# Optimization experiments

Measured on AMD Instinct MI355X. Metric: run time of the kernel, lower is better.

## Reference

```python
import jax, jax.numpy as jnp
import numpy as np

UNITS = 1024
INPUT_DIM = 512
BATCH = 2048

def setup_inputs() -> dict:
    key = jax.random.key(0)
    k1, k2, k3, k4 = jax.random.split(key, 4)
    return {
        "inputs": jax.random.normal(k1, (BATCH, INPUT_DIM), dtype=jnp.float32),
        "h_tm1": jax.random.normal(k2, (BATCH, UNITS), dtype=jnp.float32),
        "c_tm1": jax.random.normal(k3, (BATCH, UNITS), dtype=jnp.float32),
        # keras 'random_normal' initializer: stddev 0.05
        "kernel": jax.random.normal(k4, (UNITS + INPUT_DIM, 4 * UNITS), dtype=jnp.float32) * 0.05,
    }

def reference(inputs, h_tm1, c_tm1, kernel):
    # z = concat([h, x]) @ kernel ; kernel rows: [units (h-block); input_dim (x-block)]
    z = jnp.concatenate([h_tm1, inputs], axis=-1) @ kernel  # [B, 4*units]
    z0, z1, z2, z3 = jnp.split(z, 4, axis=-1)
    i = jax.nn.sigmoid(z0)
    f = jax.nn.sigmoid(z1)
    c_tilde = jnp.tanh(z2)
    o = jax.nn.sigmoid(z3)
    c = f * c_tm1 + i * c_tilde
    h = o * jnp.tanh(c)
    return (h, c)
```

## Files before the change

kernel.cpp:

```cpp
#include <hip/hip_runtime.h>
#include <hip/hip_bf16.h>
#include <stdint.h>

#define UNITS 1024
#define IDIM  512
#define BATCH 2048
#define KTOT  1536
#define NGATE 4096
#define BK    64
#define NITER (KTOT / BK)

typedef short bf16x8 __attribute__((ext_vector_type(8)));
typedef float f32x4  __attribute__((ext_vector_type(4)));

#define AS3(p) ((__attribute__((address_space(3))) void*)(p))
#define AS1(p) ((const __attribute__((address_space(1))) void*)(p))

union P8 { bf16x8 v; __hip_bfloat16 e[8]; };

#define NBLK_A 1536
#define NBLK_T 3072

__global__ __launch_bounds__(256) void prep(
    const float* __restrict__ x, const float* __restrict__ h,
    const float* __restrict__ W,
    __hip_bfloat16* __restrict__ A, __hip_bfloat16* __restrict__ Wt) {
  __shared__ float tile[32][65];
  const int tid = threadIdx.x;
  if (blockIdx.x < NBLK_A) {
    const int id = blockIdx.x * 256 + tid;
    const int r = id / (KTOT / 8);
    const int k = (id % (KTOT / 8)) * 8;
    const float* src = (k < UNITS) ? h + (size_t)r * UNITS + k
                                   : x + (size_t)r * IDIM + (k - UNITS);
    const float4 v0 = ((const float4*)src)[0];
    const float4 v1 = ((const float4*)src)[1];
    P8 o;
    o.e[0] = __float2bfloat16(v0.x); o.e[1] = __float2bfloat16(v0.y);
    o.e[2] = __float2bfloat16(v0.z); o.e[3] = __float2bfloat16(v0.w);
    o.e[4] = __float2bfloat16(v1.x); o.e[5] = __float2bfloat16(v1.y);
    o.e[6] = __float2bfloat16(v1.z); o.e[7] = __float2bfloat16(v1.w);
    *(bf16x8*)(A + (size_t)r * KTOT + k) = o.v;
  } else {
    const int b  = blockIdx.x - NBLK_A;
    const int kb = b >> 7;
    const int nb = b & 127;
    const int k0 = kb * 64, n0 = nb * 32;
    const int n4 = (tid & 7) * 4;
    const int kk = tid >> 3;
#pragma unroll
    for (int rr = 0; rr < 64; rr += 32) {
      const float4 v = *(const float4*)(W + (size_t)(k0 + kk + rr) * NGATE + n0 + n4);
      tile[n4 + 0][kk + rr] = v.x; tile[n4 + 1][kk + rr] = v.y;
      tile[n4 + 2][kk + rr] = v.z; tile[n4 + 3][kk + rr] = v.w;
    }
    __syncthreads();
    const int n  = tid >> 3;
    const int k8 = (tid & 7) * 8;
    P8 o;
#pragma unroll
    for (int j = 0; j < 8; ++j) o.e[j] = __float2bfloat16(tile[n][k8 + j]);
    *(bf16x8*)(Wt + (size_t)(n0 + n) * KTOT + k0 + k8) = o.v;
  }
}

__global__ __launch_bounds__(256, 2) void lstm_gemm(
    const __hip_bfloat16* __restrict__ A,
    const __hip_bfloat16* __restrict__ Wt,
    const float* __restrict__ c_tm1,
    float* __restrict__ out) {
  __shared__ __attribute__((aligned(128))) char lds[4 * 16384];

  const int tid  = threadIdx.x;
  const int w    = tid >> 6;
  const int lane = tid & 63;
  const int quad = lane >> 4;
  const int m16  = lane & 15;
  const int wr   = w >> 1;
  const int wu   = w & 1;

  const int mb = blockIdx.x >> 5;
  const int ub = blockIdx.x & 31;
  const int m0 = mb * 128;
  const int u0 = ub * 32;

  const __hip_bfloat16* ptr[8];
  int dst[8];
#pragma unroll
  for (int s = 0; s < 8; ++s) {
    const int q  = s * 4 + w;
    const int ci = (q & 15) * 64 + lane;
    const int row = ci >> 3;
    const int k8  = (ci & 7) ^ (row & 7);
    if (q < 16) {
      ptr[s] = A + (size_t)(m0 + row) * KTOT + k8 * 8;
      dst[s] = q * 1024;
    } else {
      const int wrow = ((row >> 5) << 10) + u0 + (row & 31);
      ptr[s] = Wt + (size_t)wrow * KTOT + k8 * 8;
      dst[s] = 32768 + (q - 16) * 1024;
    }
  }

  f32x4 acc[4][4];
#pragma unroll
  for (int i = 0; i < 4; ++i)
#pragma unroll
    for (int g = 0; g < 4; ++g) {
      f32x4 z = {0.f, 0.f, 0.f, 0.f};
      acc[i][g] = z;
    }

#pragma unroll
  for (int s = 0; s < 8; ++s)
    __builtin_amdgcn_global_load_lds(AS1(ptr[s]), AS3(lds + dst[s]), 16, 0, 0);
  __syncthreads();

  for (int it = 0; it < NITER; ++it) {
    const int cur = it & 1;
    const int nxt = cur ^ 1;
    if (it < NITER - 1) {
      const int koff = (it + 1) * BK;
#pragma unroll
      for (int s = 0; s < 8; ++s)
        __builtin_amdgcn_global_load_lds(AS1(ptr[s] + koff),
                                         AS3(lds + dst[s] + nxt * 16384), 16, 0, 0);
    }
    const char* abuf = lds + cur * 16384;
    const char* bbuf = lds + 32768 + cur * 16384;
#pragma unroll
    for (int t = 0; t < 2; ++t) {
      bf16x8 a[4], b[4];
#pragma unroll
      for (int i = 0; i < 4; ++i) {
        const int row  = wr * 64 + i * 16 + m16;
        const int slot = (t * 4 + quad) ^ (row & 7);
        a[i] = *(const bf16x8*)(abuf + (row * 8 + slot) * 16);
      }
#pragma unroll
      for (int g = 0; g < 4; ++g) {
        const int vr   = g * 32 + wu * 16 + m16;
        const int slot = (t * 4 + quad) ^ (vr & 7);
        b[g] = *(const bf16x8*)(bbuf + (vr * 8 + slot) * 16);
      }
#pragma unroll
      for (int g = 0; g < 4; ++g)
#pragma unroll
        for (int i = 0; i < 4; ++i)
          acc[i][g] = __builtin_amdgcn_mfma_f32_16x16x32_bf16(a[i], b[g], acc[i][g], 0, 0, 0);
    }
    __syncthreads();
  }

  const int u = u0 + wu * 16 + m16;
#pragma unroll
  for (int i = 0; i < 4; ++i)
#pragma unroll
    for (int reg = 0; reg < 4; ++reg) {
      const int r = m0 + wr * 64 + i * 16 + quad * 4 + reg;
      const float z0 = acc[i][0][reg];
      const float z1 = acc[i][1][reg];
      const float z2 = acc[i][2][reg];
      const float z3 = acc[i][3][reg];
      const float ig = 1.f / (1.f + __expf(-z0));
      const float fg = 1.f / (1.f + __expf(-z1));
      const float ct = 1.f - 2.f / (__expf(2.f * z2) + 1.f);
      const float og = 1.f / (1.f + __expf(-z3));
      const float cc = fg * c_tm1[(size_t)r * UNITS + u] + ig * ct;
      const float hh = og * (1.f - 2.f / (__expf(2.f * cc) + 1.f));
      out[(size_t)r * UNITS + u] = hh;
      out[(size_t)BATCH * UNITS + (size_t)r * UNITS + u] = cc;
    }
}

__global__ __launch_bounds__(256) void lstm_naive(
    const float* __restrict__ x, const float* __restrict__ h,
    const float* __restrict__ c_tm1, const float* __restrict__ W,
    float* __restrict__ out) {
  int idx = blockIdx.x * 256 + threadIdx.x;
  int r = idx / UNITS;
  int u = idx % UNITS;
  float z[4] = {0.f, 0.f, 0.f, 0.f};
  for (int k = 0; k < KTOT; ++k) {
    float a = (k < UNITS) ? h[(size_t)r * UNITS + k] : x[(size_t)r * IDIM + k - UNITS];
#pragma unroll
    for (int g = 0; g < 4; ++g)
      z[g] += a * W[(size_t)k * NGATE + g * UNITS + u];
  }
  float ig = 1.f / (1.f + __expf(-z[0]));
  float fg = 1.f / (1.f + __expf(-z[1]));
  float ct = 1.f - 2.f / (__expf(2.f * z[2]) + 1.f);
  float og = 1.f / (1.f + __expf(-z[3]));
  float cc = fg * c_tm1[(size_t)r * UNITS + u] + ig * ct;
  float hh = og * (1.f - 2.f / (__expf(2.f * cc) + 1.f));
  out[(size_t)r * UNITS + u] = hh;
  out[(size_t)BATCH * UNITS + (size_t)r * UNITS + u] = cc;
}

extern "C" void kernel_launch(void* const* d_in, const int* in_sizes, int n_in,
                              void* d_out, int out_size, void* d_ws, size_t ws_size,
                              hipStream_t stream) {
  const float* x = (const float*)d_in[0];
  const float* h = (const float*)d_in[1];
  const float* c = (const float*)d_in[2];
  const float* W = (const float*)d_in[3];
  float* out = (float*)d_out;

  const size_t needA  = (size_t)BATCH * KTOT * sizeof(__hip_bfloat16);
  const size_t needWt = (size_t)NGATE * KTOT * sizeof(__hip_bfloat16);
  if (ws_size < needA + needWt) {
    hipLaunchKernelGGL(lstm_naive, dim3((BATCH * UNITS) / 256), dim3(256), 0, stream,
                       x, h, c, W, out);
    return;
  }

  __hip_bfloat16* A  = (__hip_bfloat16*)d_ws;
  __hip_bfloat16* Wt = (__hip_bfloat16*)((char*)d_ws + needA);

  hipLaunchKernelGGL(prep, dim3(NBLK_A + NBLK_T), dim3(256), 0, stream, x, h, W, A, Wt);
  hipLaunchKernelGGL(lstm_gemm, dim3(512), dim3(256), 0, stream, A, Wt, c, out);
}
```

Measured before the change: 120.8 us.

## Split K-tile into half-stages with vmcnt waits, new swizzle, prefetch c_tm1

The 64-wide K tile is split into two 32-wide halves in LDS with a 4-slot XOR swizzle. Loads are issued per half, and partial s_waitcnt vmcnt plus barriers replace the full __syncthreads, so the next half-tile's loads overlap the MFMAs on the current half. MFMA sections are wrapped in s_setprio, and the c_tm1 values for the epilogue are loaded before the final compute steps to hide their latency. The hand-written waitcnt counts and the LDS buffer reuse make correctness depend on exact load ordering.

```diff
diff --git a/kernel.cpp b/kernel.cpp
--- a/kernel.cpp
+++ b/kernel.cpp
@@ -84,23 +84,37 @@
   const int m0 = mb * 128;
   const int u0 = ub * 32;
 
-  const __hip_bfloat16* ptr[8];
-  int dst[8];
-#pragma unroll
-  for (int s = 0; s < 8; ++s) {
+  const __hip_bfloat16* ptr[4];
+  int dst[4];
+#pragma unroll
+  for (int s = 0; s < 4; ++s) {
     const int q  = s * 4 + w;
-    const int ci = (q & 15) * 64 + lane;
-    const int row = ci >> 3;
-    const int k8  = (ci & 7) ^ (row & 7);
-    if (q < 16) {
+    const int ci = (q & 7) * 64 + lane;
+    const int row = ci >> 2;
+    const int sl  = ci & 3;
+    const int xs  = (row & 3) ^ ((row >> 2) & 3);
+    const int k8  = sl ^ xs;
+    if (q < 8) {
       ptr[s] = A + (size_t)(m0 + row) * KTOT + k8 * 8;
       dst[s] = q * 1024;
     } else {
       const int wrow = ((row >> 5) << 10) + u0 + (row & 31);
       ptr[s] = Wt + (size_t)wrow * KTOT + k8 * 8;
-      dst[s] = 32768 + (q - 16) * 1024;
-    }
-  }
+      dst[s] = 32768 + (q - 8) * 1024;
+    }
+  }
+
+  auto issue = [&](int koffE, int ldsOff) {
+#pragma unroll
+    for (int s = 0; s < 4; ++s)
+      __builtin_amdgcn_global_load_lds(AS1(ptr[s] + koffE),
+                                       AS3(lds + dst[s] + ldsOff), 16, 0, 0);
+  };
+
+  const int x16  = (m16 & 3) ^ ((m16 >> 2) & 3);
+  const int sA   = quad ^ x16;
+  const int aoff = (wr * 64 + m16) * 64 + sA * 16;
+  const int boff = 32768 + (wu * 16 + m16) * 64 + sA * 16;
 
   f32x4 acc[4][4];
 #pragma unroll
@@ -111,48 +125,59 @@
       acc[i][g] = z;
     }
 
-#pragma unroll
-  for (int s = 0; s < 8; ++s)
-    __builtin_amdgcn_global_load_lds(AS1(ptr[s]), AS3(lds + dst[s]), 16, 0, 0);
-  __syncthreads();
-
-  for (int it = 0; it < NITER; ++it) {
-    const int cur = it & 1;
-    const int nxt = cur ^ 1;
-    if (it < NITER - 1) {
-      const int koff = (it + 1) * BK;
-#pragma unroll
-      for (int s = 0; s < 8; ++s)
-        __builtin_amdgcn_global_load_lds(AS1(ptr[s] + koff),
-                                         AS3(lds + dst[s] + nxt * 16384), 16, 0, 0);
-    }
-    const char* abuf = lds + cur * 16384;
-    const char* bbuf = lds + 32768 + cur * 16384;
-#pragma unroll
-    for (int t = 0; t < 2; ++t) {
-      bf16x8 a[4], b[4];
-#pragma unroll
-      for (int i = 0; i < 4; ++i) {
-        const int row  = wr * 64 + i * 16 + m16;
-        const int slot = (t * 4 + quad) ^ (row & 7);
-        a[i] = *(const bf16x8*)(abuf + (row * 8 + slot) * 16);
-      }
-#pragma unroll
-      for (int g = 0; g < 4; ++g) {
-        const int vr   = g * 32 + wu * 16 + m16;
-        const int slot = (t * 4 + quad) ^ (vr & 7);
-        b[g] = *(const bf16x8*)(bbuf + (vr * 8 + slot) * 16);
-      }
-#pragma unroll
-      for (int g = 0; g < 4; ++g)
-#pragma unroll
-        for (int i = 0; i < 4; ++i)
-          acc[i][g] = __builtin_amdgcn_mfma_f32_16x16x32_bf16(a[i], b[g], acc[i][g], 0, 0, 0);
-    }
-    __syncthreads();
+  auto compute = [&](int coff) {
+    bf16x8 a[4], b[4];
+    const char* ab = lds + coff + aoff;
+    const char* bb = lds + coff + boff;
+#pragma unroll
+    for (int i = 0; i < 4; ++i) a[i] = *(const bf16x8*)(ab + i * 1024);
+#pragma unroll
+    for (int g = 0; g < 4; ++g) b[g] = *(const bf16x8*)(bb + g * 2048);
+    __builtin_amdgcn_s_setprio(1);
+#pragma unroll
+    for (int g = 0; g < 4; ++g)
+#pragma unroll
+      for (int i = 0; i < 4; ++i)
+        acc[i][g] = __builtin_amdgcn_mfma_f32_16x16x32_bf16(a[i], b[g], acc[i][g], 0, 0, 0);
+    __builtin_amdgcn_s_setprio(0);
+  };
+
+#define WAITB(N)                                          \
+  asm volatile("s_waitcnt vmcnt(" #N ")" ::: "memory");   \
+  __builtin_amdgcn_s_barrier();                           \
+  asm volatile("" ::: "memory");
+
+  issue(0, 0);
+  issue(32, 8192);
+
+  for (int it = 0; it < NITER - 1; ++it) {
+    const int coff = (it & 1) * 16384;
+    const int noff = coff ^ 16384;
+    const int ke   = (it + 1) * BK;
+    issue(ke, noff);
+    WAITB(8)
+    issue(ke + 32, noff + 8192);
+    compute(coff);
+    WAITB(8)
+    compute(coff + 8192);
   }
 
   const int u = u0 + wu * 16 + m16;
+  float cpre[4][4];
+#pragma unroll
+  for (int i = 0; i < 4; ++i)
+#pragma unroll
+    for (int reg = 0; reg < 4; ++reg) {
+      const int r = m0 + wr * 64 + i * 16 + quad * 4 + reg;
+      cpre[i][reg] = c_tm1[(size_t)r * UNITS + u];
+    }
+  WAITB(20)
+  compute(((NITER - 1) & 1) * 16384);
+  WAITB(16)
+  compute(((NITER - 1) & 1) * 16384 + 8192);
+
+#undef WAITB
+
 #pragma unroll
   for (int i = 0; i < 4; ++i)
 #pragma unroll
@@ -166,7 +191,7 @@
       const float fg = 1.f / (1.f + __expf(-z1));
       const float ct = 1.f - 2.f / (__expf(2.f * z2) + 1.f);
       const float og = 1.f / (1.f + __expf(-z3));
-      const float cc = fg * c_tm1[(size_t)r * UNITS + u] + ig * ct;
+      const float cc = fg * cpre[i][reg] + ig * ct;
       const float hh = og * (1.f - 2.f / (__expf(2.f * cc) + 1.f));
       out[(size_t)r * UNITS + u] = hh;
       out[(size_t)BATCH * UNITS + (size_t)r * UNITS + u] = cc;
```

After: 125.5 us. 3.9% more time.

## Double GEMM block M-tile to 256 rows and prefetch c_tm1 before final step

Applied to the files above, without the earlier changes.

The block tile grows from 128 to 256 batch rows, so each wave holds 8x4 accumulators and the grid halves to 256 blocks, one per CU. Each loaded weight tile is reused across twice as many rows, which cuts global and LDS traffic for B. The last k-iteration is peeled so the c_tm1 loads are issued before it and overlap the final MFMAs. The cost is one block per CU with heavy register use and 96KB of LDS, which lowers occupancy and latency hiding.

```diff
diff --git a/kernel.cpp b/kernel.cpp
--- a/kernel.cpp
+++ b/kernel.cpp
@@ -64,12 +64,12 @@
   }
 }
 
-__global__ __launch_bounds__(256, 2) void lstm_gemm(
+__global__ __launch_bounds__(256, 1) void lstm_gemm(
     const __hip_bfloat16* __restrict__ A,
     const __hip_bfloat16* __restrict__ Wt,
     const float* __restrict__ c_tm1,
     float* __restrict__ out) {
-  __shared__ __attribute__((aligned(128))) char lds[4 * 16384];
+  __shared__ __attribute__((aligned(128))) char lds[98304];
 
   const int tid  = threadIdx.x;
   const int w    = tid >> 6;
@@ -81,62 +81,54 @@
 
   const int mb = blockIdx.x >> 5;
   const int ub = blockIdx.x & 31;
-  const int m0 = mb * 128;
+  const int m0 = mb * 256;
   const int u0 = ub * 32;
 
-  const __hip_bfloat16* ptr[8];
-  int dst[8];
-#pragma unroll
-  for (int s = 0; s < 8; ++s) {
-    const int q  = s * 4 + w;
-    const int ci = (q & 15) * 64 + lane;
-    const int row = ci >> 3;
-    const int k8  = (ci & 7) ^ (row & 7);
-    if (q < 16) {
+  const __hip_bfloat16* ptr[12];
+  int dst[12];
+#pragma unroll
+  for (int s = 0; s < 12; ++s) {
+    const int q = s * 4 + w;
+    if (s < 8) {
+      const int ci  = q * 64 + lane;
+      const int row = ci >> 3;
+      const int k8  = (ci & 7) ^ (row & 7);
       ptr[s] = A + (size_t)(m0 + row) * KTOT + k8 * 8;
       dst[s] = q * 1024;
     } else {
-      const int wrow = ((row >> 5) << 10) + u0 + (row & 31);
+      const int qb  = q - 32;
+      const int cb  = qb * 64 + lane;
+      const int vr  = cb >> 3;
+      const int k8  = (cb & 7) ^ (vr & 7);
+      const int wrow = ((vr >> 5) << 10) + u0 + (vr & 31);
       ptr[s] = Wt + (size_t)wrow * KTOT + k8 * 8;
-      dst[s] = 32768 + (q - 16) * 1024;
-    }
-  }
-
-  f32x4 acc[4][4];
-#pragma unroll
-  for (int i = 0; i < 4; ++i)
+      dst[s] = 65536 + qb * 1024;
+    }
+  }
+
+  f32x4 acc[8][4];
+#pragma unroll
+  for (int i = 0; i < 8; ++i)
 #pragma unroll
     for (int g = 0; g < 4; ++g) {
       f32x4 z = {0.f, 0.f, 0.f, 0.f};
       acc[i][g] = z;
     }
 
-#pragma unroll
-  for (int s = 0; s < 8; ++s)
-    __builtin_amdgcn_global_load_lds(AS1(ptr[s]), AS3(lds + dst[s]), 16, 0, 0);
-  __syncthreads();
-
-  for (int it = 0; it < NITER; ++it) {
-    const int cur = it & 1;
-    const int nxt = cur ^ 1;
-    if (it < NITER - 1) {
-      const int koff = (it + 1) * BK;
-#pragma unroll
-      for (int s = 0; s < 8; ++s)
-        __builtin_amdgcn_global_load_lds(AS1(ptr[s] + koff),
-                                         AS3(lds + dst[s] + nxt * 16384), 16, 0, 0);
-    }
-    const char* abuf = lds + cur * 16384;
-    const char* bbuf = lds + 32768 + cur * 16384;
+  auto issue = [&](int koffE, int nxt) {
+#pragma unroll
+    for (int s = 0; s < 12; ++s) {
+      const int off = dst[s] + ((s < 8) ? nxt * 32768 : nxt * 16384);
+      __builtin_amdgcn_global_load_lds(AS1(ptr[s] + koffE), AS3(lds + off), 16, 0, 0);
+    }
+  };
+
+  auto compute = [&](int cur) {
+    const char* abuf = lds + cur * 32768;
+    const char* bbuf = lds + 65536 + cur * 16384;
 #pragma unroll
     for (int t = 0; t < 2; ++t) {
-      bf16x8 a[4], b[4];
-#pragma unroll
-      for (int i = 0; i < 4; ++i) {
-        const int row  = wr * 64 + i * 16 + m16;
-        const int slot = (t * 4 + quad) ^ (row & 7);
-        a[i] = *(const bf16x8*)(abuf + (row * 8 + slot) * 16);
-      }
+      bf16x8 a[8], b[4];
 #pragma unroll
       for (int g = 0; g < 4; ++g) {
         const int vr   = g * 32 + wu * 16 + m16;
@@ -144,20 +136,45 @@
         b[g] = *(const bf16x8*)(bbuf + (vr * 8 + slot) * 16);
       }
 #pragma unroll
+      for (int i = 0; i < 8; ++i) {
+        const int row  = wr * 128 + i * 16 + m16;
+        const int slot = (t * 4 + quad) ^ (row & 7);
+        a[i] = *(const bf16x8*)(abuf + (row * 8 + slot) * 16);
+      }
+#pragma unroll
       for (int g = 0; g < 4; ++g)
 #pragma unroll
-        for (int i = 0; i < 4; ++i)
+        for (int i = 0; i < 8; ++i)
           acc[i][g] = __builtin_amdgcn_mfma_f32_16x16x32_bf16(a[i], b[g], acc[i][g], 0, 0, 0);
     }
+  };
+
+  issue(0, 0);
+  __syncthreads();
+
+  for (int it = 0; it < NITER - 1; ++it) {
+    issue((it + 1) * BK, (it + 1) & 1);
+    compute(it & 1);
     __syncthreads();
   }
 
   const int u = u0 + wu * 16 + m16;
-#pragma unroll
-  for (int i = 0; i < 4; ++i)
+  float cpre[8][4];
+#pragma unroll
+  for (int i = 0; i < 8; ++i)
 #pragma unroll
     for (int reg = 0; reg < 4; ++reg) {
-      const int r = m0 + wr * 64 + i * 16 + quad * 4 + reg;
+      const int r = m0 + wr * 128 + i * 16 + quad * 4 + reg;
+      cpre[i][reg] = c_tm1[(size_t)r * UNITS + u];
+    }
+
+  compute((NITER - 1) & 1);
+
+#pragma unroll
+  for (int i = 0; i < 8; ++i)
+#pragma unroll
+    for (int reg = 0; reg < 4; ++reg) {
+      const int r = m0 + wr * 128 + i * 16 + quad * 4 + reg;
       const float z0 = acc[i][0][reg];
       const float z1 = acc[i][1][reg];
       const float z2 = acc[i][2][reg];
@@ -166,7 +183,7 @@
       const float fg = 1.f / (1.f + __expf(-z1));
       const float ct = 1.f - 2.f / (__expf(2.f * z2) + 1.f);
       const float og = 1.f / (1.f + __expf(-z3));
-      const float cc = fg * c_tm1[(size_t)r * UNITS + u] + ig * ct;
+      const float cc = fg * cpre[i][reg] + ig * ct;
       const float hh = og * (1.f - 2.f / (__expf(2.f * cc) + 1.f));
       out[(size_t)r * UNITS + u] = hh;
       out[(size_t)BATCH * UNITS + (size_t)r * UNITS + u] = cc;
@@ -218,5 +235,5 @@
   __hip_bfloat16* Wt = (__hip_bfloat16*)((char*)d_ws + needA);
 
   hipLaunchKernelGGL(prep, dim3(NBLK_A + NBLK_T), dim3(256), 0, stream, x, h, W, A, Wt);
-  hipLaunchKernelGGL(lstm_gemm, dim3(512), dim3(256), 0, stream, A, Wt, c, out);
-}
+  hipLaunchKernelGGL(lstm_gemm, dim3(256), dim3(256), 0, stream, A, Wt, c, out);
+}
```

After: 132.7 us. 9.9% more time.

## Fuse prep and GEMM into one cooperative kernel with grid sync

Applied to the files above, without the earlier changes.

Merges the bf16 conversion/transpose prep and the MFMA GEMM into a single cooperative kernel. Each of 512 blocks runs 9 prep tasks, then a grid-wide barrier precedes the GEMM phase. This removes one kernel launch and the inter-kernel gap. In exchange, prep now runs on only 512 blocks instead of 4608, and the grid sync adds cost. Falls back to the two-kernel path if the cooperative launch fails.

```diff
diff --git a/kernel.cpp b/kernel.cpp
--- a/kernel.cpp
+++ b/kernel.cpp
@@ -1,4 +1,5 @@
 #include <hip/hip_runtime.h>
+#include <hip/hip_cooperative_groups.h>
 #include <hip/hip_bf16.h>
 #include <stdint.h>
 
@@ -18,60 +19,73 @@
 
 union P8 { bf16x8 v; __hip_bfloat16 e[8]; };
 
-#define NBLK_A 1536
-#define NBLK_T 3072
-
-__global__ __launch_bounds__(256) void prep(
+#define NTASK_A 1536
+#define NTASK_W 3072
+#define NTASK   (NTASK_A + NTASK_W)
+
+__device__ __forceinline__ void a_task(int task, int tid,
+    const float* x, const float* h, __hip_bfloat16* A) {
+  const int id = task * 256 + tid;
+  const int r = id / (KTOT / 8);
+  const int k = (id % (KTOT / 8)) * 8;
+  const float* src = (k < UNITS) ? h + (size_t)r * UNITS + k
+                                 : x + (size_t)r * IDIM + (k - UNITS);
+  const float4 v0 = ((const float4*)src)[0];
+  const float4 v1 = ((const float4*)src)[1];
+  P8 o;
+  o.e[0] = __float2bfloat16(v0.x); o.e[1] = __float2bfloat16(v0.y);
+  o.e[2] = __float2bfloat16(v0.z); o.e[3] = __float2bfloat16(v0.w);
+  o.e[4] = __float2bfloat16(v1.x); o.e[5] = __float2bfloat16(v1.y);
+  o.e[6] = __float2bfloat16(v1.z); o.e[7] = __float2bfloat16(v1.w);
+  *(bf16x8*)(A + (size_t)r * KTOT + k) = o.v;
+}
+
+__device__ __forceinline__ void w_task(int b, int tid,
+    const float* W, __hip_bfloat16* Wt, float (*tile)[65]) {
+  const int kb = b >> 7;
+  const int nb = b & 127;
+  const int k0 = kb * 64, n0 = nb * 32;
+  const int n4 = (tid & 7) * 4;
+  const int kk = tid >> 3;
+#pragma unroll
+  for (int rr = 0; rr < 64; rr += 32) {
+    const float4 v = *(const float4*)(W + (size_t)(k0 + kk + rr) * NGATE + n0 + n4);
+    tile[n4 + 0][kk + rr] = v.x; tile[n4 + 1][kk + rr] = v.y;
+    tile[n4 + 2][kk + rr] = v.z; tile[n4 + 3][kk + rr] = v.w;
+  }
+  __syncthreads();
+  const int n  = tid >> 3;
+  const int k8 = (tid & 7) * 8;
+  P8 o;
+#pragma unroll
+  for (int j = 0; j < 8; ++j) o.e[j] = __float2bfloat16(tile[n][k8 + j]);
+  *(bf16x8*)(Wt + (size_t)(n0 + n) * KTOT + k0 + k8) = o.v;
+}
+
+__global__ __launch_bounds__(256, 2) void lstm_all(
     const float* __restrict__ x, const float* __restrict__ h,
-    const float* __restrict__ W,
-    __hip_bfloat16* __restrict__ A, __hip_bfloat16* __restrict__ Wt) {
-  __shared__ float tile[32][65];
+    const float* __restrict__ W, const float* __restrict__ c_tm1,
+    __hip_bfloat16* A, __hip_bfloat16* Wt, float* out) {
+  __shared__ __attribute__((aligned(128))) char lds[4 * 16384];
+
   const int tid = threadIdx.x;
-  if (blockIdx.x < NBLK_A) {
-    const int id = blockIdx.x * 256 + tid;
-    const int r = id / (KTOT / 8);
-    const int k = (id % (KTOT / 8)) * 8;
-    const float* src = (k < UNITS) ? h + (size_t)r * UNITS + k
-                                   : x + (size_t)r * IDIM + (k - UNITS);
-    const float4 v0 = ((const float4*)src)[0];
-    const float4 v1 = ((const float4*)src)[1];
-    P8 o;
-    o.e[0] = __float2bfloat16(v0.x); o.e[1] = __float2bfloat16(v0.y);
-    o.e[2] = __float2bfloat16(v0.z); o.e[3] = __float2bfloat16(v0.w);
-    o.e[4] = __float2bfloat16(v1.x); o.e[5] = __float2bfloat16(v1.y);
-    o.e[6] = __float2bfloat16(v1.z); o.e[7] = __float2bfloat16(v1.w);
-    *(bf16x8*)(A + (size_t)r * KTOT + k) = o.v;
-  } else {
-    const int b  = blockIdx.x - NBLK_A;
-    const int kb = b >> 7;
-    const int nb = b & 127;
-    const int k0 = kb * 64, n0 = nb * 32;
-    const int n4 = (tid & 7) * 4;
-    const int kk = tid >> 3;
-#pragma unroll
-    for (int rr = 0; rr < 64; rr += 32) {
-      const float4 v = *(const float4*)(W + (size_t)(k0 + kk + rr) * NGATE + n0 + n4);
-      tile[n4 + 0][kk + rr] = v.x; tile[n4 + 1][kk + rr] = v.y;
-      tile[n4 + 2][kk + rr] = v.z; tile[n4 + 3][kk + rr] = v.w;
-    }
-    __syncthreads();
-    const int n  = tid >> 3;
-    const int k8 = (tid & 7) * 8;
-    P8 o;
-#pragma unroll
-    for (int j = 0; j < 8; ++j) o.e[j] = __float2bfloat16(tile[n][k8 + j]);
-    *(bf16x8*)(Wt + (size_t)(n0 + n) * KTOT + k0 + k8) = o.v;
-  }
-}
-
-__global__ __launch_bounds__(256, 2) void lstm_gemm(
-    const __hip_bfloat16* __restrict__ A,
-    const __hip_bfloat16* __restrict__ Wt,
-    const float* __restrict__ c_tm1,
-    float* __restrict__ out) {
-  __shared__ __attribute__((aligned(128))) char lds[4 * 16384];
-
-  const int tid  = threadIdx.x;
+
+  {
+    float (*tile)[65] = (float (*)[65])lds;
+#pragma unroll 1
+    for (int t9 = 0; t9 < 9; ++t9) {
+      const int task = blockIdx.x * 9 + t9;
+      if (task < NTASK_A) {
+        a_task(task, tid, x, h, A);
+      } else {
+        __syncthreads();
+        w_task(task - NTASK_A, tid, W, Wt, tile);
+      }
+    }
+  }
+  __threadfence();
+  cooperative_groups::this_grid().sync();
+
   const int w    = tid >> 6;
   const int lane = tid & 63;
   const int quad = lane >> 4;
@@ -173,6 +187,125 @@
     }
 }
 
+__global__ __launch_bounds__(256) void prep(
+    const float* __restrict__ x, const float* __restrict__ h,
+    const float* __restrict__ W,
+    __hip_bfloat16* __restrict__ A, __hip_bfloat16* __restrict__ Wt) {
+  __shared__ float tile[32][65];
+  const int tid = threadIdx.x;
+  if (blockIdx.x < NTASK_A) a_task(blockIdx.x, tid, x, h, A);
+  else                      w_task(blockIdx.x - NTASK_A, tid, W, Wt, tile);
+}
+
+__global__ __launch_bounds__(256, 2) void lstm_gemm(
+    const __hip_bfloat16* __restrict__ A,
+    const __hip_bfloat16* __restrict__ Wt,
+    const float* __restrict__ c_tm1,
+    float* __restrict__ out) {
+  __shared__ __attribute__((aligned(128))) char lds[4 * 16384];
+
+  const int tid  = threadIdx.x;
+  const int w    = tid >> 6;
+  const int lane = tid & 63;
+  const int quad = lane >> 4;
+  const int m16  = lane & 15;
+  const int wr   = w >> 1;
+  const int wu   = w & 1;
+
+  const int mb = blockIdx.x >> 5;
+  const int ub = blockIdx.x & 31;
+  const int m0 = mb * 128;
+  const int u0 = ub * 32;
+
+  const __hip_bfloat16* ptr[8];
+  int dst[8];
+#pragma unroll
+  for (int s = 0; s < 8; ++s) {
+    const int q  = s * 4 + w;
+    const int ci = (q & 15) * 64 + lane;
+    const int row = ci >> 3;
+    const int k8  = (ci & 7) ^ (row & 7);
+    if (q < 16) {
+      ptr[s] = A + (size_t)(m0 + row) * KTOT + k8 * 8;
+      dst[s] = q * 1024;
+    } else {
+      const int wrow = ((row >> 5) << 10) + u0 + (row & 31);
+      ptr[s] = Wt + (size_t)wrow * KTOT + k8 * 8;
+      dst[s] = 32768 + (q - 16) * 1024;
+    }
+  }
+
+  f32x4 acc[4][4];
+#pragma unroll
+  for (int i = 0; i < 4; ++i)
+#pragma unroll
+    for (int g = 0; g < 4; ++g) {
+      f32x4 z = {0.f, 0.f, 0.f, 0.f};
+      acc[i][g] = z;
+    }
+
+#pragma unroll
+  for (int s = 0; s < 8; ++s)
+    __builtin_amdgcn_global_load_lds(AS1(ptr[s]), AS3(lds + dst[s]), 16, 0, 0);
+  __syncthreads();
+
+  for (int it = 0; it < NITER; ++it) {
+    const int cur = it & 1;
+    const int nxt = cur ^ 1;
+    if (it < NITER - 1) {
+      const int koff = (it + 1) * BK;
+#pragma unroll
+      for (int s = 0; s < 8; ++s)
+        __builtin_amdgcn_global_load_lds(AS1(ptr[s] + koff),
+                                         AS3(lds + dst[s] + nxt * 16384), 16, 0, 0);
+    }
+    const char* abuf = lds + cur * 16384;
+    const char* bbuf = lds + 32768 + cur * 16384;
+#pragma unroll
+    for (int t = 0; t < 2; ++t) {
+      bf16x8 a[4], b[4];
+#pragma unroll
+      for (int i = 0; i < 4; ++i) {
+        const int row  = wr * 64 + i * 16 + m16;
+        const int slot = (t * 4 + quad) ^ (row & 7);
+        a[i] = *(const bf16x8*)(abuf + (row * 8 + slot) * 16);
+      }
+#pragma unroll
+      for (int g = 0; g < 4; ++g) {
+        const int vr   = g * 32 + wu * 16 + m16;
+        const int slot = (t * 4 + quad) ^ (vr & 7);
+        b[g] = *(const bf16x8*)(bbuf + (vr * 8 + slot) * 16);
+      }
+#pragma unroll
+      for (int g = 0; g < 4; ++g)
+#pragma unroll
+        for (int i = 0; i < 4; ++i)
+          acc[i][g] = __builtin_amdgcn_mfma_f32_16x16x32_bf16(a[i], b[g], acc[i][g], 0, 0, 0);
+    }
+    __syncthreads();
+  }
+
+  const int u = u0 + wu * 16 + m16;
+#pragma unroll
+  for (int i = 0; i < 4; ++i)
+#pragma unroll
+    for (int reg = 0; reg < 4; ++reg) {
+      const int r = m0 + wr * 64 + i * 16 + quad * 4 + reg;
+      const float z0 = acc[i][0][reg];
+      const float z1 = acc[i][1][reg];
+      const float z2 = acc[i][2][reg];
+      const float z3 = acc[i][3][reg];
+      const float ig = 1.f / (1.f + __expf(-z0));
+      const float fg = 1.f / (1.f + __expf(-z1));
+      const float ct = 1.f - 2.f / (__expf(2.f * z2) + 1.f);
+      const float og = 1.f / (1.f + __expf(-z3));
+      const float cc = fg * c_tm1[(size_t)r * UNITS + u] + ig * ct;
+      const float hh = og * (1.f - 2.f / (__expf(2.f * cc) + 1.f));
+      out[(size_t)r * UNITS + u] = hh;
+      out[(size_t)BATCH * UNITS + (size_t)r * UNITS + u] = cc;
+    }
+}
+
 __global__ __launch_bounds__(256) void lstm_naive(
     const float* __restrict__ x, const float* __restrict__ h,
     const float* __restrict__ c_tm1, const float* __restrict__ W,
@@ -217,6 +350,13 @@
   __hip_bfloat16* A  = (__hip_bfloat16*)d_ws;
   __hip_bfloat16* Wt = (__hip_bfloat16*)((char*)d_ws + needA);
 
-  hipLaunchKernelGGL(prep, dim3(NBLK_A + NBLK_T), dim3(256), 0, stream, x, h, W, A, Wt);
-  hipLaunchKernelGGL(lstm_gemm, dim3(512), dim3(256), 0, stream, A, Wt, c, out);
-}
+  void* args[7] = {(void*)&x, (void*)&h, (void*)&W, (void*)&c,
+                   (void*)&A, (void*)&Wt, (void*)&out};
+  hipError_t e = hipLaunchCooperativeKernel((void*)lstm_all, dim3(512), dim3(256),
+                                            args, 0, stream);
+  if (e != hipSuccess) {
+    (void)hipGetLastError();
+    hipLaunchKernelGGL(prep, dim3(NTASK), dim3(256), 0, stream, x, h, W, A, Wt);
+    hipLaunchKernelGGL(lstm_gemm, dim3(512), dim3(256), 0, stream, A, Wt, c, out);
+  }
+}
```

Result: slower. 262.4 us (+117.3%).
